# Optimization experiments

Hardware: AMD Instinct MI355X
Metric: run time of the kernel (lower is better)

Reference implementation:

```python
import jax, jax.numpy as jnp
import numpy as np
import math

DIM = 1024
H = 16
DH = DIM // H
B = 2
L = 1024


def setup_inputs() -> dict:
    key = jax.random.key(0)
    ks = jax.random.split(key, 8)
    s = 1.0 / math.sqrt(DIM)
    return {
        "Q": jax.random.normal(ks[0], (B, L, DIM), jnp.float32),
        "K": jax.random.normal(ks[1], (B, L, DIM), jnp.float32),
        "mask_Q": jax.random.bernoulli(ks[2], 0.1, (B, L)),
        "mask_K": jax.random.bernoulli(ks[3], 0.1, (B, L)),
        "Wq": jax.random.normal(ks[4], (DIM, DIM), jnp.float32) * s,
        "Wk": jax.random.normal(ks[5], (DIM, DIM), jnp.float32) * s,
        "Wv": jax.random.normal(ks[6], (DIM, DIM), jnp.float32) * s,
        "Wo": jax.random.normal(ks[7], (DIM, DIM), jnp.float32) * s,
    }


def reference(Q, K, mask_Q, mask_K, Wq, Wk, Wv, Wo):
    # V defaults to K. Masked positions of inputs are zeroed first.
    Qz = jnp.where(mask_Q[:, :, None], 0.0, Q)
    Kz = jnp.where(mask_K[:, :, None], 0.0, K)
    Vz = Kz  # V = K, masked with mask_K

    # Projections (nn.Linear, no bias): y = x @ W.T
    Qp = jnp.einsum('bld,ed->ble', Qz, Wq)
    Kp = jnp.einsum('bld,ed->ble', Kz, Wk)
    Vp = jnp.einsum('bld,ed->ble', Vz, Wv)

    # split heads: [B, L, H, DH] -> per-head attention
    qh = Qp.reshape(B, L, H, DH)
    kh = Kp.reshape(B, L, H, DH)
    vh = Vp.reshape(B, L, H, DH)

    # NOTE: original scales by sqrt(dim) (full dim), not sqrt(dim_split)
    scores = jnp.einsum('bqhd,bkhd->bhqk', qh, kh) / math.sqrt(DIM)

    # outer-product validity mask: valid iff both q and k positions unmasked
    valid = (~mask_Q)[:, None, :, None] & (~mask_K)[:, None, None, :]  # [B,1,Lq,Lk]
    A = jnp.where(valid, scores, -1e38)
    A = jax.nn.softmax(A, axis=-1)
    A = jnp.where(valid, A, 0.0)

    O = jnp.einsum('bhqk,bkhd->bqhd', A, vh).reshape(B, L, DIM)
    # residual uses the PROJECTED Q (Q was reassigned to fc_q(Q) in torch)
    O = Qp + O
    # masked_forward(fc_o, ...): fc_o applied, masked query rows forced to 0
    ff = jax.nn.relu(jnp.where(mask_Q[:, :, None], 0.0, jnp.einsum('bld,ed->ble', O, Wo)))
    O = O + ff
    return O
```

## Files before the change

### kernel.cpp

```cpp
#include <hip/hip_runtime.h>
#include <hip/hip_bf16.h>


#define DEV __device__ __forceinline__

typedef __attribute__((ext_vector_type(8))) short bf16x8;
typedef __attribute__((ext_vector_type(4))) float f32x4;
typedef __hip_bfloat16 bf16;

DEV void glds16(const bf16* g, bf16* s) {
  __builtin_amdgcn_global_load_lds(
      (const __attribute__((address_space(1))) void*)g,
      (__attribute__((address_space(3))) void*)s, 16, 0, 0);
}

DEV unsigned short f2bu(float x) {
  __hip_bfloat16 b = __float2bfloat16(x);
  unsigned short u;
  __builtin_memcpy(&u, &b, 2);
  return u;
}

DEV float bu2f(unsigned short u) {
  unsigned int v = (unsigned int)u << 16;
  float f;
  __builtin_memcpy(&f, &v, 4);
  return f;
}

__global__ void normalize_masks(const unsigned char* mq_raw, const unsigned char* mk_raw,
                                unsigned char* outq, unsigned char* outk,
                                unsigned long long* qm64, unsigned long long* km64) {
  __shared__ int cnt;
  int t = threadIdx.x;
  if (t == 0) cnt = 0;
  __syncthreads();
  int c = 0;
  for (int i = t; i < 2048; i += 256) c += (mq_raw[i] != 0);
  atomicAdd(&cnt, c);
  __syncthreads();
  bool isByte = cnt > 128;
  for (int i = t; i < 2048; i += 256) {
    unsigned char q, k;
    if (isByte) {
      q = (mq_raw[i] != 0); k = (mk_raw[i] != 0);
    } else {
      q = (((const int*)mq_raw)[i] != 0); k = (((const int*)mk_raw)[i] != 0);
    }
    outq[i] = q; outk[i] = k;
  }
  __syncthreads();
  if (t < 64) {
    const unsigned char* src = (t < 32) ? outk : outq;
    int idx = t & 31;
    unsigned long long m = 0;
    for (int j = 0; j < 64; ++j)
      m |= (unsigned long long)(src[idx * 64 + j] != 0) << j;
    if (t < 32) km64[idx] = m; else qm64[idx] = m;
  }
}

__global__ __launch_bounds__(256) void cast_all(
    const float* __restrict__ Q, const float* __restrict__ K,
    const unsigned char* __restrict__ mq, const unsigned char* __restrict__ mk,
    const float* __restrict__ W0, const float* __restrict__ W1,
    const float* __restrict__ W2, const float* __restrict__ W3,
    bf16* __restrict__ Qz, bf16* __restrict__ Kz,
    bf16* __restrict__ o0, bf16* __restrict__ o1,
    bf16* __restrict__ o2, bf16* __restrict__ o3) {
  const int z = blockIdx.z;
  if (z < 2) {
    const float* X = z ? K : Q;
    const unsigned char* m = z ? mk : mq;
    bf16* out = z ? Kz : Qz;
    int i = (blockIdx.x * 256 + threadIdx.x) * 8;
    float4 v0 = *(const float4*)&X[i];
    float4 v1 = *(const float4*)&X[i + 4];
    if (m[i >> 10]) {
      v0 = make_float4(0.f, 0.f, 0.f, 0.f);
      v1 = make_float4(0.f, 0.f, 0.f, 0.f);
    }
    *(ushort4*)&out[i] = make_ushort4(f2bu(v0.x), f2bu(v0.y), f2bu(v0.z), f2bu(v0.w));
    *(ushort4*)&out[i + 4] = make_ushort4(f2bu(v1.x), f2bu(v1.y), f2bu(v1.z), f2bu(v1.w));
  } else {
    const float* X; bf16* out;
    switch (z) {
      case 2: X = W0; out = o0; break;
      case 3: X = W1; out = o1; break;
      case 4: X = W2; out = o2; break;
      default: X = W3; out = o3; break;
    }
    int i = (blockIdx.x * 256 + threadIdx.x) * 4;
    float4 v = *(const float4*)&X[i];
    *(ushort4*)&out[i] = make_ushort4(f2bu(v.x), f2bu(v.y), f2bu(v.z), f2bu(v.w));
  }
}

template <int MI, int NI, typename EPI>
DEV void gemm_core(const bf16* __restrict__ A, const bf16* __restrict__ W,
                   int K, int brow, int bcol, EPI&& epi) {
  __shared__ bf16 As[2 * MI * 512];
  __shared__ bf16 Bs[2 * NI * 2048];
  const int t = threadIdx.x, l = t & 63, w = t >> 6;
  const int rs = l >> 2;
  const int kcol = (l & 3) * 8;

  f32x4 acc[MI][NI];
#pragma unroll
  for (int i = 0; i < MI; i++)
#pragma unroll
    for (int j = 0; j < NI; j++) acc[i][j] = (f32x4){0.f, 0.f, 0.f, 0.f};

  auto stage = [&](int k0, int b_) {
#pragma unroll
    for (int i = 0; i < MI; ++i)
      if ((i & 3) == w)
        glds16(A + (size_t)(brow + i * 16 + rs) * K + k0 + kcol,
               &As[b_ * MI * 512 + i * 512]);
#pragma unroll
    for (int c = 0; c < NI; ++c)
      glds16(W + (size_t)(bcol + (w * NI + c) * 16 + rs) * K + k0 + kcol,
             &Bs[b_ * NI * 2048 + (w * NI + c) * 512]);
  };

  const int aoff0 = (l & 15) * 32 + (l >> 4) * 8;
  const int boff0 = (w * NI * 16 + (l & 15)) * 32 + (l >> 4) * 8;

  stage(0, 0);
  int buf = 0;
  for (int k0 = 0; k0 < K; k0 += 32) {
    __syncthreads();
    if (k0 + 32 < K) stage(k0 + 32, buf ^ 1);
    bf16x8 a[MI], b[NI];
#pragma unroll
    for (int mi = 0; mi < MI; ++mi)
      a[mi] = *(const bf16x8*)&As[buf * MI * 512 + aoff0 + mi * 512];
#pragma unroll
    for (int ni = 0; ni < NI; ++ni)
      b[ni] = *(const bf16x8*)&Bs[buf * NI * 2048 + boff0 + ni * 512];
#pragma unroll
    for (int mi = 0; mi < MI; ++mi)
#pragma unroll
      for (int ni = 0; ni < NI; ++ni)
        acc[mi][ni] = __builtin_amdgcn_mfma_f32_16x16x32_bf16(a[mi], b[ni], acc[mi][ni], 0, 0, 0);
    buf ^= 1;
  }

#pragma unroll
  for (int mi = 0; mi < MI; ++mi)
#pragma unroll
    for (int ni = 0; ni < NI; ++ni)
#pragma unroll
      for (int r = 0; r < 4; ++r) {
        int row = brow + mi * 16 + (l >> 4) * 4 + r;
        int col = bcol + (w * NI + ni) * 16 + (l & 15);
        epi(row, col, acc[mi][ni][r]);
      }
}

__global__ __launch_bounds__(256) void proj_gemm(
    const bf16* __restrict__ Qz, const bf16* __restrict__ Kz,
    const bf16* __restrict__ Wq, const bf16* __restrict__ Wk, const bf16* __restrict__ Wv,
    bf16* __restrict__ Qpb, bf16* __restrict__ Kpb, bf16* __restrict__ Vpb) {
  const int z = blockIdx.z;
  const int brow = blockIdx.x * 64, bcol = blockIdx.y * 128;
  const bf16* A = (z == 0) ? Qz : Kz;
  const bf16* W = (z == 0) ? Wq : ((z == 1) ? Wk : Wv);
  bf16* dst = (z == 0) ? Qpb : ((z == 1) ? Kpb : Vpb);
  const float scale = (z == 0) ? 0.045084220f : 1.0f;
  gemm_core<4, 2>(A, W, 1024, brow, bcol, [&](int row, int col, float v) {
    dst[((size_t)row << 10) + col] = __float2bfloat16(v * scale);
  });
}

__global__ __launch_bounds__(256) void final_gemm(
    const bf16* __restrict__ Ob, const bf16* __restrict__ Wo,
    float* __restrict__ out, const unsigned char* __restrict__ mq) {
  const int brow = blockIdx.x * 64, bcol = blockIdx.y * 64;
  gemm_core<4, 1>(Ob, Wo, 1024, brow, bcol, [&](int row, int col, float v) {
    size_t idx = ((size_t)row << 10) + col;
    float ff = mq[row] ? 0.f : fmaxf(v, 0.f);
    out[idx] = out[idx] + ff;
  });
}

__global__ __launch_bounds__(256) void attn_fused(
    const bf16* __restrict__ Qpb, const bf16* __restrict__ Kpb, const bf16* __restrict__ Vpb,
    const unsigned long long* __restrict__ qm64, const unsigned long long* __restrict__ km64,
    float* __restrict__ Of, bf16* __restrict__ Ob) {
  __shared__ bf16 Klds[2][64 * 64];
  __shared__ bf16 Vt[64 * 72];

  const int t = threadIdx.x, l = t & 63, w = t >> 6;
  const int q = l & 15, g = l >> 4;
  const int f = blockIdx.x;
  const int bh = (f & 7) + 8 * ((f >> 3) & 3);
  const int qt = f >> 5;
  const int b = bh >> 4, h = bh & 15;
  const size_t bbase = (size_t)b * 1024;

  const int qg = qt * 64 + w * 16 + q;
  const bf16* qptr = Qpb + (bbase + qg) * 1024 + h * 64 + g * 8;
  const bf16x8 qb0 = *(const bf16x8*)qptr;
  const bf16x8 qb1 = *(const bf16x8*)(qptr + 32);

  float psum = 0.f;
  f32x4 oacc[4];
#pragma unroll
  for (int mf = 0; mf < 4; ++mf) oacc[mf] = (f32x4){0.f, 0.f, 0.f, 0.f};

  const int krow_s = l >> 3;
  const int kcol_s = ((l & 7) ^ krow_s) * 8;
  const int vk0 = 2 * (t & 31);
  const int vdc = t >> 5;

  union { uint4 v; unsigned short s[8]; } u0, u1;

  auto stageK = [&](int kt_, int b_) {
#pragma unroll
    for (int c = 0; c < 2; ++c) {
      int cw = w * 2 + c;
      glds16(Kpb + (bbase + kt_ * 64 + cw * 8 + krow_s) * 1024 + h * 64 + kcol_s,
             &Klds[b_][cw * 512]);
    }
  };
  auto loadV = [&](int kt_) {
    const bf16* g0 = Vpb + (bbase + kt_ * 64 + vk0) * 1024 + h * 64 + vdc * 8;
    u0.v = *(const uint4*)g0;
    u1.v = *(const uint4*)(g0 + 1024);
  };

  stageK(0, 0);
  loadV(0);
  int buf = 0;

  for (int kt = 0; kt < 16; ++kt) {
    const unsigned long long km = km64[b * 16 + kt];
    const unsigned long long mloc = km >> (4 * g);

    __syncthreads();

#pragma unroll
    for (int j = 0; j < 8; ++j) {
      unsigned int pk = (unsigned int)u0.s[j] | ((unsigned int)u1.s[j] << 16);
      *(unsigned int*)((char*)Vt + (vdc * 8 + j) * 144 + vk0 * 2) = pk;
    }

    f32x4 S[4];
#pragma unroll
    for (int mf = 0; mf < 4; ++mf) {
#pragma unroll
      for (int r = 0; r < 4; ++r)
        S[mf][r] = ((mloc >> (mf * 16 + r)) & 1ull) ? -1e30f : 0.f;
      const int row = mf * 16 + q;
      const int rowb = row * 128;
      const bf16x8 ka0 = *(const bf16x8*)((const char*)&Klds[buf][0] + rowb + ((g ^ (row & 7)) * 16));
      const bf16x8 ka1 = *(const bf16x8*)((const char*)&Klds[buf][0] + rowb + (((g + 4) ^ (row & 7)) * 16));
      S[mf] = __builtin_amdgcn_mfma_f32_16x16x32_bf16(ka0, qb0, S[mf], 0, 0, 0);
      S[mf] = __builtin_amdgcn_mfma_f32_16x16x32_bf16(ka1, qb1, S[mf], 0, 0, 0);
    }

    unsigned int lo[4], hi[4];
#pragma unroll
    for (int mf = 0; mf < 4; ++mf) {
      float p0 = exp2f(S[mf][0]), p1 = exp2f(S[mf][1]);
      float p2 = exp2f(S[mf][2]), p3 = exp2f(S[mf][3]);
      psum += (p0 + p1) + (p2 + p3);
      lo[mf] = (unsigned int)f2bu(p0) | ((unsigned int)f2bu(p1) << 16);
      hi[mf] = (unsigned int)f2bu(p2) | ((unsigned int)f2bu(p3) << 16);
    }

    __syncthreads();

    if (kt < 15) {
      stageK(kt + 1, buf ^ 1);
      loadV(kt + 1);
    }

    const int srcA = ((2 * g) & 3) * 16 + q;
    const int srcB = srcA + 16;
    const bool sel = (g >> 1) & 1;
#pragma unroll
    for (int ks = 0; ks < 2; ++ks) {
      unsigned int a0 = __shfl(lo[2 * ks], srcA), a1 = __shfl(hi[2 * ks], srcA);
      unsigned int a2 = __shfl(lo[2 * ks], srcB), a3 = __shfl(hi[2 * ks], srcB);
      unsigned int b0 = __shfl(lo[2 * ks + 1], srcA), b1 = __shfl(hi[2 * ks + 1], srcA);
      unsigned int b2 = __shfl(lo[2 * ks + 1], srcB), b3 = __shfl(hi[2 * ks + 1], srcB);
      uint4 pw;
      pw.x = sel ? b0 : a0; pw.y = sel ? b1 : a1;
      pw.z = sel ? b2 : a2; pw.w = sel ? b3 : a3;
      const bf16x8 pa = __builtin_bit_cast(bf16x8, pw);
#pragma unroll
      for (int mf = 0; mf < 4; ++mf) {
        const bf16x8 va = *(const bf16x8*)((const char*)Vt + (mf * 16 + q) * 144 + ks * 64 + g * 16);
        oacc[mf] = __builtin_amdgcn_mfma_f32_16x16x32_bf16(va, pa, oacc[mf], 0, 0, 0);
      }
    }
    buf ^= 1;
  }

  psum += __shfl_xor(psum, 16);
  psum += __shfl_xor(psum, 32);

  const unsigned long long qm = qm64[b * 16 + qt];
  const bool qvalid = !((qm >> (w * 16 + q)) & 1ull);
  const float inv = (qvalid && psum > 0.f) ? 1.f / psum : 0.f;
  const float RQ = 22.180709777918f;
#pragma unroll
  for (int mf = 0; mf < 4; ++mf) {
    size_t idx = (bbase + qg) * 1024 + h * 64 + mf * 16 + g * 4;
    ushort4 q4 = *(const ushort4*)&Qpb[idx];
    float4 val;
    val.x = bu2f(q4.x) * RQ + oacc[mf][0] * inv;
    val.y = bu2f(q4.y) * RQ + oacc[mf][1] * inv;
    val.z = bu2f(q4.z) * RQ + oacc[mf][2] * inv;
    val.w = bu2f(q4.w) * RQ + oacc[mf][3] * inv;
    *(float4*)&Of[idx] = val;
    *(ushort4*)&Ob[idx] = make_ushort4(f2bu(val.x), f2bu(val.y), f2bu(val.z), f2bu(val.w));
  }
}

extern "C" void kernel_launch(void* const* d_in, const int* in_sizes, int n_in,
                              void* d_out, int out_size, void* d_ws, size_t ws_size,
                              hipStream_t stream) {
  const float* Q = (const float*)d_in[0];
  const float* K = (const float*)d_in[1];
  const unsigned char* mQraw = (const unsigned char*)d_in[2];
  const unsigned char* mKraw = (const unsigned char*)d_in[3];
  const float* Wq = (const float*)d_in[4];
  const float* Wk = (const float*)d_in[5];
  const float* Wv = (const float*)d_in[6];
  const float* Wo = (const float*)d_in[7];
  float* out = (float*)d_out;

  char* ws = (char*)d_ws;
  const size_t MB = 1024 * 1024;
  bf16* Qz = (bf16*)(ws + 0);
  bf16* Kz = (bf16*)(ws + 4 * MB);
  bf16* Wqb = (bf16*)(ws + 8 * MB);
  bf16* Wkb = (bf16*)(ws + 10 * MB);
  bf16* Wvb = (bf16*)(ws + 12 * MB);
  bf16* Wob = (bf16*)(ws + 14 * MB);
  bf16* Qpb = (bf16*)(ws + 16 * MB);
  bf16* Kpb = (bf16*)(ws + 20 * MB);
  bf16* Vpb = (bf16*)(ws + 24 * MB);
  bf16* Ob  = (bf16*)(ws + 28 * MB);
  unsigned char* mqn = (unsigned char*)(ws + 32 * MB);
  unsigned char* mkn = mqn + 2048;
  unsigned long long* km64 = (unsigned long long*)(ws + 32 * MB + 4096);
  unsigned long long* qm64 = km64 + 32;

  normalize_masks<<<1, 256, 0, stream>>>(mQraw, mKraw, mqn, mkn, qm64, km64);

  dim3 gc(1024, 1, 6);
  cast_all<<<gc, 256, 0, stream>>>(Q, K, mqn, mkn, Wq, Wk, Wv, Wo,
                                   Qz, Kz, Wqb, Wkb, Wvb, Wob);

  dim3 gp(32, 8, 3);
  proj_gemm<<<gp, 256, 0, stream>>>(Qz, Kz, Wqb, Wkb, Wvb, Qpb, Kpb, Vpb);

  attn_fused<<<512, 256, 0, stream>>>(Qpb, Kpb, Vpb, qm64, km64, out, Ob);

  dim3 gf(32, 16);
  final_gemm<<<gf, 256, 0, stream>>>(Ob, Wob, out, mqn);
}
```

Before: 96.54 us.

## Fold mask normalization into cast kernel, halve GEMM tiles, split attention keys

Removes the separate mask-normalization launch by computing the mask format and bitmasks inside the cast kernel. Each Q/K cast block recounts the raw mask to detect byte versus int format, and weight casting now uses 8 elements per thread. The projection and final GEMMs halve the row tile (MI 4 to 2) so twice as many blocks launch. Attention blocks grow to 512 threads, with two groups each handling half of the key tiles and combining partial outputs and sums through LDS. This trades extra LDS use and redundant mask counting for more parallelism and one fewer launch.

```diff
diff --git a/kernel.cpp b/kernel.cpp
--- a/kernel.cpp
+++ b/kernel.cpp
@@ -28,61 +28,44 @@
   return f;
 }
 
-__global__ void normalize_masks(const unsigned char* mq_raw, const unsigned char* mk_raw,
-                                unsigned char* outq, unsigned char* outk,
-                                unsigned long long* qm64, unsigned long long* km64) {
-  __shared__ int cnt;
-  int t = threadIdx.x;
-  if (t == 0) cnt = 0;
-  __syncthreads();
-  int c = 0;
-  for (int i = t; i < 2048; i += 256) c += (mq_raw[i] != 0);
-  atomicAdd(&cnt, c);
-  __syncthreads();
-  bool isByte = cnt > 128;
-  for (int i = t; i < 2048; i += 256) {
-    unsigned char q, k;
-    if (isByte) {
-      q = (mq_raw[i] != 0); k = (mk_raw[i] != 0);
-    } else {
-      q = (((const int*)mq_raw)[i] != 0); k = (((const int*)mk_raw)[i] != 0);
-    }
-    outq[i] = q; outk[i] = k;
-  }
-  __syncthreads();
-  if (t < 64) {
-    const unsigned char* src = (t < 32) ? outk : outq;
-    int idx = t & 31;
-    unsigned long long m = 0;
-    for (int j = 0; j < 64; ++j)
-      m |= (unsigned long long)(src[idx * 64 + j] != 0) << j;
-    if (t < 32) km64[idx] = m; else qm64[idx] = m;
-  }
-}
-
 __global__ __launch_bounds__(256) void cast_all(
     const float* __restrict__ Q, const float* __restrict__ K,
-    const unsigned char* __restrict__ mq, const unsigned char* __restrict__ mk,
+    const unsigned char* __restrict__ mq_raw, const unsigned char* __restrict__ mk_raw,
     const float* __restrict__ W0, const float* __restrict__ W1,
     const float* __restrict__ W2, const float* __restrict__ W3,
     bf16* __restrict__ Qz, bf16* __restrict__ Kz,
     bf16* __restrict__ o0, bf16* __restrict__ o1,
-    bf16* __restrict__ o2, bf16* __restrict__ o3) {
+    bf16* __restrict__ o2, bf16* __restrict__ o3,
+    unsigned char* __restrict__ mqn,
+    unsigned long long* __restrict__ qm64, unsigned long long* __restrict__ km64) {
+  __shared__ int cnt;
   const int z = blockIdx.z;
+  const int t = threadIdx.x;
   if (z < 2) {
     const float* X = z ? K : Q;
-    const unsigned char* m = z ? mk : mq;
+    const unsigned char* raw = z ? mk_raw : mq_raw;
     bf16* out = z ? Kz : Qz;
-    int i = (blockIdx.x * 256 + threadIdx.x) * 8;
+    if (t == 0) cnt = 0;
+    __syncthreads();
+    int c = 0;
+#pragma unroll
+    for (int j = 0; j < 8; ++j) c += (raw[t * 8 + j] != 0);
+    atomicAdd(&cnt, c);
+    __syncthreads();
+    const bool isByte = cnt > 128;
+    int i = (blockIdx.x * 256 + t) * 8;
+    int row = i >> 10;
+    bool masked = isByte ? (raw[row] != 0) : (((const int*)raw)[row] != 0);
     float4 v0 = *(const float4*)&X[i];
     float4 v1 = *(const float4*)&X[i + 4];
-    if (m[i >> 10]) {
+    if (masked) {
       v0 = make_float4(0.f, 0.f, 0.f, 0.f);
       v1 = make_float4(0.f, 0.f, 0.f, 0.f);
     }
     *(ushort4*)&out[i] = make_ushort4(f2bu(v0.x), f2bu(v0.y), f2bu(v0.z), f2bu(v0.w));
     *(ushort4*)&out[i + 4] = make_ushort4(f2bu(v1.x), f2bu(v1.y), f2bu(v1.z), f2bu(v1.w));
-  } else {
+  } else if (z < 6) {
+    if (blockIdx.x >= 512) return;
     const float* X; bf16* out;
     switch (z) {
       case 2: X = W0; out = o0; break;
@@ -90,9 +73,33 @@
       case 4: X = W2; out = o2; break;
       default: X = W3; out = o3; break;
     }
-    int i = (blockIdx.x * 256 + threadIdx.x) * 4;
-    float4 v = *(const float4*)&X[i];
-    *(ushort4*)&out[i] = make_ushort4(f2bu(v.x), f2bu(v.y), f2bu(v.z), f2bu(v.w));
+    int i = (blockIdx.x * 256 + t) * 8;
+    float4 v0 = *(const float4*)&X[i];
+    float4 v1 = *(const float4*)&X[i + 4];
+    *(ushort4*)&out[i] = make_ushort4(f2bu(v0.x), f2bu(v0.y), f2bu(v0.z), f2bu(v0.w));
+    *(ushort4*)&out[i + 4] = make_ushort4(f2bu(v1.x), f2bu(v1.y), f2bu(v1.z), f2bu(v1.w));
+  } else {
+    if (blockIdx.x != 0) return;
+    if (t == 0) cnt = 0;
+    __syncthreads();
+    int c = 0;
+    for (int i = t; i < 2048; i += 256) c += (mq_raw[i] != 0);
+    atomicAdd(&cnt, c);
+    __syncthreads();
+    const bool isByte = cnt > 128;
+    for (int i = t; i < 2048; i += 256)
+      mqn[i] = isByte ? (mq_raw[i] != 0) : (((const int*)mq_raw)[i] != 0);
+    if (t < 64) {
+      const unsigned char* src = (t < 32) ? mk_raw : mq_raw;
+      int idx = t & 31;
+      unsigned long long m = 0;
+      for (int j = 0; j < 64; ++j) {
+        int pos = idx * 64 + j;
+        bool bit = isByte ? (src[pos] != 0) : (((const int*)src)[pos] != 0);
+        m |= (unsigned long long)bit << j;
+      }
+      if (t < 32) km64[idx] = m; else qm64[idx] = m;
+    }
   }
 }
 
@@ -163,12 +170,12 @@
     const bf16* __restrict__ Wq, const bf16* __restrict__ Wk, const bf16* __restrict__ Wv,
     bf16* __restrict__ Qpb, bf16* __restrict__ Kpb, bf16* __restrict__ Vpb) {
   const int z = blockIdx.z;
-  const int brow = blockIdx.x * 64, bcol = blockIdx.y * 128;
+  const int brow = blockIdx.x * 32, bcol = blockIdx.y * 128;
   const bf16* A = (z == 0) ? Qz : Kz;
   const bf16* W = (z == 0) ? Wq : ((z == 1) ? Wk : Wv);
   bf16* dst = (z == 0) ? Qpb : ((z == 1) ? Kpb : Vpb);
   const float scale = (z == 0) ? 0.045084220f : 1.0f;
-  gemm_core<4, 2>(A, W, 1024, brow, bcol, [&](int row, int col, float v) {
+  gemm_core<2, 2>(A, W, 1024, brow, bcol, [&](int row, int col, float v) {
     dst[((size_t)row << 10) + col] = __float2bfloat16(v * scale);
   });
 }
@@ -176,22 +183,26 @@
 __global__ __launch_bounds__(256) void final_gemm(
     const bf16* __restrict__ Ob, const bf16* __restrict__ Wo,
     float* __restrict__ out, const unsigned char* __restrict__ mq) {
-  const int brow = blockIdx.x * 64, bcol = blockIdx.y * 64;
-  gemm_core<4, 1>(Ob, Wo, 1024, brow, bcol, [&](int row, int col, float v) {
+  const int brow = blockIdx.x * 32, bcol = blockIdx.y * 64;
+  gemm_core<2, 1>(Ob, Wo, 1024, brow, bcol, [&](int row, int col, float v) {
     size_t idx = ((size_t)row << 10) + col;
     float ff = mq[row] ? 0.f : fmaxf(v, 0.f);
     out[idx] = out[idx] + ff;
   });
 }
 
-__global__ __launch_bounds__(256) void attn_fused(
+__global__ __launch_bounds__(512) void attn_fused(
     const bf16* __restrict__ Qpb, const bf16* __restrict__ Kpb, const bf16* __restrict__ Vpb,
     const unsigned long long* __restrict__ qm64, const unsigned long long* __restrict__ km64,
     float* __restrict__ Of, bf16* __restrict__ Ob) {
-  __shared__ bf16 Klds[2][64 * 64];
-  __shared__ bf16 Vt[64 * 72];
+  __shared__ bf16 Klds[2][2][64 * 64];
+  __shared__ bf16 Vt[2][64 * 72];
+  __shared__ float CombO[256][17];
+  __shared__ float CombP[256];
 
   const int t = threadIdx.x, l = t & 63, w = t >> 6;
+  const int kg = w >> 2, wq = w & 3;
+  const int tg = t & 255;
   const int q = l & 15, g = l >> 4;
   const int f = blockIdx.x;
   const int bh = (f & 7) + 8 * ((f >> 3) & 3);
@@ -199,7 +210,7 @@
   const int b = bh >> 4, h = bh & 15;
   const size_t bbase = (size_t)b * 1024;
 
-  const int qg = qt * 64 + w * 16 + q;
+  const int qg = qt * 64 + wq * 16 + q;
   const bf16* qptr = Qpb + (bbase + qg) * 1024 + h * 64 + g * 8;
   const bf16x8 qb0 = *(const bf16x8*)qptr;
   const bf16x8 qb1 = *(const bf16x8*)(qptr + 32);
@@ -211,17 +222,17 @@
 
   const int krow_s = l >> 3;
   const int kcol_s = ((l & 7) ^ krow_s) * 8;
-  const int vk0 = 2 * (t & 31);
-  const int vdc = t >> 5;
+  const int vk0 = 2 * (tg & 31);
+  const int vdc = tg >> 5;
 
   union { uint4 v; unsigned short s[8]; } u0, u1;
 
   auto stageK = [&](int kt_, int b_) {
 #pragma unroll
     for (int c = 0; c < 2; ++c) {
-      int cw = w * 2 + c;
+      int cw = wq * 2 + c;
       glds16(Kpb + (bbase + kt_ * 64 + cw * 8 + krow_s) * 1024 + h * 64 + kcol_s,
-             &Klds[b_][cw * 512]);
+             &Klds[kg][b_][cw * 512]);
     }
   };
   auto loadV = [&](int kt_) {
@@ -230,11 +241,12 @@
     u1.v = *(const uint4*)(g0 + 1024);
   };
 
-  stageK(0, 0);
-  loadV(0);
+  stageK(kg * 8, 0);
+  loadV(kg * 8);
   int buf = 0;
 
-  for (int kt = 0; kt < 16; ++kt) {
+  for (int it = 0; it < 8; ++it) {
+    const int kt = kg * 8 + it;
     const unsigned long long km = km64[b * 16 + kt];
     const unsigned long long mloc = km >> (4 * g);
 
@@ -243,7 +255,7 @@
 #pragma unroll
     for (int j = 0; j < 8; ++j) {
       unsigned int pk = (unsigned int)u0.s[j] | ((unsigned int)u1.s[j] << 16);
-      *(unsigned int*)((char*)Vt + (vdc * 8 + j) * 144 + vk0 * 2) = pk;
+      *(unsigned int*)((char*)&Vt[kg][0] + (vdc * 8 + j) * 144 + vk0 * 2) = pk;
     }
 
     f32x4 S[4];
@@ -254,8 +266,8 @@
         S[mf][r] = ((mloc >> (mf * 16 + r)) & 1ull) ? -1e30f : 0.f;
       const int row = mf * 16 + q;
       const int rowb = row * 128;
-      const bf16x8 ka0 = *(const bf16x8*)((const char*)&Klds[buf][0] + rowb + ((g ^ (row & 7)) * 16));
-      const bf16x8 ka1 = *(const bf16x8*)((const char*)&Klds[buf][0] + rowb + (((g + 4) ^ (row & 7)) * 16));
+      const bf16x8 ka0 = *(const bf16x8*)((const char*)&Klds[kg][buf][0] + rowb + ((g ^ (row & 7)) * 16));
+      const bf16x8 ka1 = *(const bf16x8*)((const char*)&Klds[kg][buf][0] + rowb + (((g + 4) ^ (row & 7)) * 16));
       S[mf] = __builtin_amdgcn_mfma_f32_16x16x32_bf16(ka0, qb0, S[mf], 0, 0, 0);
       S[mf] = __builtin_amdgcn_mfma_f32_16x16x32_bf16(ka1, qb1, S[mf], 0, 0, 0);
     }
@@ -272,7 +284,7 @@
 
     __syncthreads();
 
-    if (kt < 15) {
+    if (it < 7) {
       stageK(kt + 1, buf ^ 1);
       loadV(kt + 1);
     }
@@ -292,31 +304,47 @@
       const bf16x8 pa = __builtin_bit_cast(bf16x8, pw);
 #pragma unroll
       for (int mf = 0; mf < 4; ++mf) {
-        const bf16x8 va = *(const bf16x8*)((const char*)Vt + (mf * 16 + q) * 144 + ks * 64 + g * 16);
+        const bf16x8 va = *(const bf16x8*)((const char*)&Vt[kg][0] + (mf * 16 + q) * 144 + ks * 64 + g * 16);
         oacc[mf] = __builtin_amdgcn_mfma_f32_16x16x32_bf16(va, pa, oacc[mf], 0, 0, 0);
       }
     }
     buf ^= 1;
   }
 
-  psum += __shfl_xor(psum, 16);
-  psum += __shfl_xor(psum, 32);
-
-  const unsigned long long qm = qm64[b * 16 + qt];
-  const bool qvalid = !((qm >> (w * 16 + q)) & 1ull);
-  const float inv = (qvalid && psum > 0.f) ? 1.f / psum : 0.f;
-  const float RQ = 22.180709777918f;
-#pragma unroll
-  for (int mf = 0; mf < 4; ++mf) {
-    size_t idx = (bbase + qg) * 1024 + h * 64 + mf * 16 + g * 4;
-    ushort4 q4 = *(const ushort4*)&Qpb[idx];
-    float4 val;
-    val.x = bu2f(q4.x) * RQ + oacc[mf][0] * inv;
-    val.y = bu2f(q4.y) * RQ + oacc[mf][1] * inv;
-    val.z = bu2f(q4.z) * RQ + oacc[mf][2] * inv;
-    val.w = bu2f(q4.w) * RQ + oacc[mf][3] * inv;
-    *(float4*)&Of[idx] = val;
-    *(ushort4*)&Ob[idx] = make_ushort4(f2bu(val.x), f2bu(val.y), f2bu(val.z), f2bu(val.w));
+  __syncthreads();
+  if (t >= 256) {
+#pragma unroll
+    for (int mf = 0; mf < 4; ++mf)
+#pragma unroll
+      for (int r = 0; r < 4; ++r) CombO[tg][mf * 4 + r] = oacc[mf][r];
+    CombP[tg] = psum;
+  }
+  __syncthreads();
+  if (t < 256) {
+#pragma unroll
+    for (int mf = 0; mf < 4; ++mf)
+#pragma unroll
+      for (int r = 0; r < 4; ++r) oacc[mf][r] += CombO[t][mf * 4 + r];
+    psum += CombP[t];
+    psum += __shfl_xor(psum, 16);
+    psum += __shfl_xor(psum, 32);
+
+    const unsigned long long qm = qm64[b * 16 + qt];
+    const bool qvalid = !((qm >> (wq * 16 + q)) & 1ull);
+    const float inv = (qvalid && psum > 0.f) ? 1.f / psum : 0.f;
+    const float RQ = 22.180709777918f;
+#pragma unroll
+    for (int mf = 0; mf < 4; ++mf) {
+      size_t idx = (bbase + qg) * 1024 + h * 64 + mf * 16 + g * 4;
+      ushort4 q4 = *(const ushort4*)&Qpb[idx];
+      float4 val;
+      val.x = bu2f(q4.x) * RQ + oacc[mf][0] * inv;
+      val.y = bu2f(q4.y) * RQ + oacc[mf][1] * inv;
+      val.z = bu2f(q4.z) * RQ + oacc[mf][2] * inv;
+      val.w = bu2f(q4.w) * RQ + oacc[mf][3] * inv;
+      *(float4*)&Of[idx] = val;
+      *(ushort4*)&Ob[idx] = make_ushort4(f2bu(val.x), f2bu(val.y), f2bu(val.z), f2bu(val.w));
+    }
   }
 }
 
@@ -346,21 +374,18 @@
   bf16* Vpb = (bf16*)(ws + 24 * MB);
   bf16* Ob  = (bf16*)(ws + 28 * MB);
   unsigned char* mqn = (unsigned char*)(ws + 32 * MB);
-  unsigned char* mkn = mqn + 2048;
   unsigned long long* km64 = (unsigned long long*)(ws + 32 * MB + 4096);
   unsigned long long* qm64 = km64 + 32;
 
-  normalize_masks<<<1, 256, 0, stream>>>(mQraw, mKraw, mqn, mkn, qm64, km64);
-
-  dim3 gc(1024, 1, 6);
-  cast_all<<<gc, 256, 0, stream>>>(Q, K, mqn, mkn, Wq, Wk, Wv, Wo,
-                                   Qz, Kz, Wqb, Wkb, Wvb, Wob);
-
-  dim3 gp(32, 8, 3);
+  dim3 gc(1024, 1, 7);
+  cast_all<<<gc, 256, 0, stream>>>(Q, K, mQraw, mKraw, Wq, Wk, Wv, Wo,
+                                   Qz, Kz, Wqb, Wkb, Wvb, Wob, mqn, qm64, km64);
+
+  dim3 gp(64, 8, 3);
   proj_gemm<<<gp, 256, 0, stream>>>(Qz, Kz, Wqb, Wkb, Wvb, Qpb, Kpb, Vpb);
 
-  attn_fused<<<512, 256, 0, stream>>>(Qpb, Kpb, Vpb, qm64, km64, out, Ob);
-
-  dim3 gf(32, 16);
+  attn_fused<<<512, 512, 0, stream>>>(Qpb, Kpb, Vpb, qm64, km64, out, Ob);
+
+  dim3 gf(64, 16);
   final_gemm<<<gf, 256, 0, stream>>>(Ob, Wob, out, mqn);
 }
```

Result: slower. 104.5 us (+8.2%).
